# Kernel tuning notes

Measured on AMD Instinct MI355X. Metric: run time of the kernel, lower is better.

Reference implementation:

```python
import jax, jax.numpy as jnp
import numpy as np

N_SITES = 100000
N_PERM = 6
N_NEIGH = 6
FEAT = 64
OUT_FEAT = 64


def setup_inputs() -> dict:
    key = jax.random.key(0)
    k1, k2, k3, k4 = jax.random.split(key, 4)
    X_sites = jax.random.normal(k1, (N_SITES, FEAT), dtype=jnp.float32)
    X_NSs = jax.random.randint(k2, (N_SITES, N_PERM, N_NEIGH), 0, N_SITES, dtype=jnp.int64)
    # Linear(input_feature=N_NEIGH*FEAT, output_feature=OUT_FEAT): weight (out, in), bias (out,)
    W = jax.random.normal(k3, (OUT_FEAT, N_NEIGH * FEAT), dtype=jnp.float32) * (1.0 / np.sqrt(N_NEIGH * FEAT))
    b = jax.random.normal(k4, (OUT_FEAT,), dtype=jnp.float32) * 0.01
    return {"X_sites": X_sites, "X_NSs": X_NSs, "N_sites": N_SITES, "W": W, "b": b}


def reference(X_sites, X_NSs, N_sites, W, b):
    # Vectorized form of the per-site Python loop:
    # for each site i: gather X_sites[X_NSs[i]] -> (P, n_neigh, feat),
    # flatten to (P, n_neigh*feat), apply Linear.
    N, P, n = X_NSs.shape
    f = X_sites.shape[1]
    gathered = X_sites[X_NSs]                      # (N, P, n, f)  irregular gather
    flat = gathered.reshape(N, P, n * f)           # (N, P, n*f)
    # Linear: y = x @ W.T + b
    out = jnp.einsum('npi,oi->npo', flat, W) + b   # (N, P, out)
    return out
```

## Files before the change

### kernel.cpp

```cpp
#include <hip/hip_runtime.h>
#include <hip/hip_fp16.h>

#define FEAT   64
#define NNEIGH 6
#define OUTF   64
#define INFEAT (NNEIGH * FEAT)

typedef __attribute__((ext_vector_type(8))) short bf16x8;
typedef __attribute__((ext_vector_type(4))) float f32x4;

__device__ __forceinline__ short bf16_hi(float v) {
  return (short)(__float_as_uint(v) >> 16);
}
__device__ __forceinline__ float bf16_rec(float v) {
  return __uint_as_float(__float_as_uint(v) & 0xffff0000u);
}

__global__ __launch_bounds__(256) void lcnn_prep(
    const float* __restrict__ W, short* __restrict__ BThi,
    short* __restrict__ BTlo) {
  const int t = blockIdx.x * 256 + threadIdx.x;
  if (t >= INFEAT * FEAT) return;
  const int j = t >> 6, f = t & 63;
  const float v = W[(size_t)(j & 63) * INFEAT + (j >> 6) * 64 + f];
  const short h = bf16_hi(v);
  const float lo = v - bf16_rec(v);
  BThi[t] = h;
  BTlo[t] = bf16_hi(lo);
}

__global__ __launch_bounds__(256) void lcnn_p1_mfma(
    const float* __restrict__ X, const short* __restrict__ BThi,
    const short* __restrict__ BTlo, __half* __restrict__ Y, int nsites) {
  __shared__ alignas(16) __half lds[4][16 * INFEAT];

  const int lane = threadIdx.x & 63;
  const int wid  = threadIdx.x >> 6;
  const int g    = lane >> 4;
  const int c    = lane & 15;
  const int m0   = (blockIdx.x * 4 + wid) * 16;

  int srow = m0 + c;
  if (srow >= nsites) srow = nsites - 1;
  const float* xr = X + (size_t)srow * FEAT;

  float af[2][8];
  *(float4*)&af[0][0] = *(const float4*)(xr + g * 8);
  *(float4*)&af[0][4] = *(const float4*)(xr + g * 8 + 4);
  *(float4*)&af[1][0] = *(const float4*)(xr + 32 + g * 8);
  *(float4*)&af[1][4] = *(const float4*)(xr + 32 + g * 8 + 4);

  bf16x8 ah[2], al[2];
#pragma unroll
  for (int ks = 0; ks < 2; ++ks)
#pragma unroll
    for (int i = 0; i < 8; ++i) {
      const float v = af[ks][i];
      ah[ks][i] = bf16_hi(v);
      al[ks][i] = bf16_hi(v - bf16_rec(v));
    }

#pragma unroll 4
  for (int nt = 0; nt < 24; ++nt) {
    const int jrow = (nt * 16 + c) * 64;
    const bf16x8 bh0 = *(const bf16x8*)(BThi + jrow + g * 8);
    const bf16x8 bh1 = *(const bf16x8*)(BThi + jrow + 32 + g * 8);
    const bf16x8 bl0 = *(const bf16x8*)(BTlo + jrow + g * 8);
    const bf16x8 bl1 = *(const bf16x8*)(BTlo + jrow + 32 + g * 8);

    f32x4 acc = {0.f, 0.f, 0.f, 0.f};
    acc = __builtin_amdgcn_mfma_f32_16x16x32_bf16(ah[0], bh0, acc, 0, 0, 0);
    acc = __builtin_amdgcn_mfma_f32_16x16x32_bf16(al[0], bh0, acc, 0, 0, 0);
    acc = __builtin_amdgcn_mfma_f32_16x16x32_bf16(ah[0], bl0, acc, 0, 0, 0);
    acc = __builtin_amdgcn_mfma_f32_16x16x32_bf16(ah[1], bh1, acc, 0, 0, 0);
    acc = __builtin_amdgcn_mfma_f32_16x16x32_bf16(al[1], bh1, acc, 0, 0, 0);
    acc = __builtin_amdgcn_mfma_f32_16x16x32_bf16(ah[1], bl1, acc, 0, 0, 0);

#pragma unroll
    for (int r = 0; r < 4; ++r)
      lds[wid][(g * 4 + r) * INFEAT + nt * 16 + c] = __float2half(acc[r]);
  }

  const int rows = min(16, nsites - m0);
  if (rows > 0) {
    const int n16 = rows * 48;
    const uint4* src = (const uint4*)&lds[wid][0];
    uint4* dst = (uint4*)((char*)Y + (size_t)m0 * (INFEAT * 2));
    for (int t = lane; t < n16; t += 64) dst[t] = src[t];
  }
}

__global__ __launch_bounds__(256) void lcnn_phase2(
    const int* __restrict__ idx, const __half* __restrict__ Y,
    const float* __restrict__ b, float* __restrict__ out, int nrows) {
  const int lane = threadIdx.x & 63;
  int row = blockIdx.x * 4 + (threadIdx.x >> 6);
  if (row >= nrows) return;
  row = __builtin_amdgcn_readfirstlane(row);

  const int* ip = idx + (size_t)row * NNEIGH;
  const int s0 = ip[0], s1 = ip[1], s2 = ip[2], s3 = ip[3], s4 = ip[4], s5 = ip[5];

  const __half y0 = Y[(size_t)s0 * INFEAT + 0 * FEAT + lane];
  const __half y1 = Y[(size_t)s1 * INFEAT + 1 * FEAT + lane];
  const __half y2 = Y[(size_t)s2 * INFEAT + 2 * FEAT + lane];
  const __half y3 = Y[(size_t)s3 * INFEAT + 3 * FEAT + lane];
  const __half y4 = Y[(size_t)s4 * INFEAT + 4 * FEAT + lane];
  const __half y5 = Y[(size_t)s5 * INFEAT + 5 * FEAT + lane];

  const float acc = b[lane]
      + ((__half2float(y0) + __half2float(y1)) + (__half2float(y2) + __half2float(y3)))
      + (__half2float(y4) + __half2float(y5));

  __builtin_nontemporal_store(acc, &out[(size_t)row * OUTF + lane]);
}

__global__ __launch_bounds__(256) void lcnn_naive(
    const float* __restrict__ X, const int* __restrict__ idx,
    const float* __restrict__ W, const float* __restrict__ b,
    float* __restrict__ out, int nrows) {
  const int lane = threadIdx.x & 63;
  int row = blockIdx.x * 4 + (threadIdx.x >> 6);
  if (row >= nrows) return;

  const int* ip = idx + (size_t)row * NNEIGH;
  float acc = b[lane];
#pragma unroll 1
  for (int k = 0; k < NNEIGH; ++k) {
    const int s = ip[k];
    const float* xr = X + (size_t)s * FEAT;
    const float* wr = W + (size_t)lane * INFEAT + k * FEAT;
#pragma unroll
    for (int f = 0; f < FEAT; ++f) acc += xr[f] * wr[f];
  }
  out[(size_t)row * OUTF + lane] = acc;
}

extern "C" void kernel_launch(void* const* d_in, const int* in_sizes, int n_in,
                              void* d_out, int out_size, void* d_ws, size_t ws_size,
                              hipStream_t stream) {
  const float* X   = (const float*)d_in[0];
  const int*   idx = (const int*)d_in[1];
  const float* W   = (const float*)d_in[3];
  const float* b   = (const float*)d_in[4];
  float*       out = (float*)d_out;

  const int nsites = in_sizes[0] / FEAT;
  const int nrows  = in_sizes[1] / NNEIGH;

  const size_t ybytes  = (size_t)nsites * INFEAT * sizeof(__half);
  const size_t btbytes = (size_t)INFEAT * FEAT * sizeof(short);
  if (ws_size >= ybytes + 2 * btbytes) {
    __half* Y    = (__half*)d_ws;
    short*  BThi = (short*)((char*)d_ws + ybytes);
    short*  BTlo = BThi + INFEAT * FEAT;

    lcnn_prep<<<(INFEAT * FEAT + 255) / 256, 256, 0, stream>>>(W, BThi, BTlo);
    lcnn_p1_mfma<<<(nsites + 63) / 64, 256, 0, stream>>>(X, BThi, BTlo, Y, nsites);
    lcnn_phase2<<<(nrows + 3) / 4, 256, 0, stream>>>(idx, Y, b, out, nrows);
  } else {
    lcnn_naive<<<(nrows + 3) / 4, 256, 0, stream>>>(X, idx, W, b, out, nrows);
  }
}
```

Measured before the change: 361.3 us.

## Drop LDS staging in projection kernel and batch gather rows per wave

The MFMA projection kernel swaps operand order so each lane holds four consecutive output columns of one site row. It then writes them straight to Y as 8-byte stores, removing the LDS staging buffer and the copy-out loop. The gather/sum kernel now has each wave handle 8 output rows. It loads all 48 indices with one coalesced load, shares them via shuffles, and issues 24 independent 4-byte half2 gathers per lane before summing. This aims for more memory-level parallelism and wider stores, in exchange for narrower, less-coalesced Y writes in the first kernel.

```diff
diff --git a/kernel.cpp b/kernel.cpp
--- a/kernel.cpp
+++ b/kernel.cpp
@@ -23,17 +23,13 @@
   if (t >= INFEAT * FEAT) return;
   const int j = t >> 6, f = t & 63;
   const float v = W[(size_t)(j & 63) * INFEAT + (j >> 6) * 64 + f];
-  const short h = bf16_hi(v);
-  const float lo = v - bf16_rec(v);
-  BThi[t] = h;
-  BTlo[t] = bf16_hi(lo);
+  BThi[t] = bf16_hi(v);
+  BTlo[t] = bf16_hi(v - bf16_rec(v));
 }
 
 __global__ __launch_bounds__(256) void lcnn_p1_mfma(
     const float* __restrict__ X, const short* __restrict__ BThi,
     const short* __restrict__ BTlo, __half* __restrict__ Y, int nsites) {
-  __shared__ alignas(16) __half lds[4][16 * INFEAT];
-
   const int lane = threadIdx.x & 63;
   const int wid  = threadIdx.x >> 6;
   const int g    = lane >> 4;
@@ -41,7 +37,8 @@
   const int m0   = (blockIdx.x * 4 + wid) * 16;
 
   int srow = m0 + c;
-  if (srow >= nsites) srow = nsites - 1;
+  const bool valid = (srow < nsites);
+  if (!valid) srow = nsites - 1;
   const float* xr = X + (size_t)srow * FEAT;
 
   float af[2][8];
@@ -50,14 +47,14 @@
   *(float4*)&af[1][0] = *(const float4*)(xr + 32 + g * 8);
   *(float4*)&af[1][4] = *(const float4*)(xr + 32 + g * 8 + 4);
 
-  bf16x8 ah[2], al[2];
+  bf16x8 xh[2], xl[2];
 #pragma unroll
   for (int ks = 0; ks < 2; ++ks)
 #pragma unroll
     for (int i = 0; i < 8; ++i) {
       const float v = af[ks][i];
-      ah[ks][i] = bf16_hi(v);
-      al[ks][i] = bf16_hi(v - bf16_rec(v));
+      xh[ks][i] = bf16_hi(v);
+      xl[ks][i] = bf16_hi(v - bf16_rec(v));
     }
 
 #pragma unroll 4
@@ -69,24 +66,18 @@
     const bf16x8 bl1 = *(const bf16x8*)(BTlo + jrow + 32 + g * 8);
 
     f32x4 acc = {0.f, 0.f, 0.f, 0.f};
-    acc = __builtin_amdgcn_mfma_f32_16x16x32_bf16(ah[0], bh0, acc, 0, 0, 0);
-    acc = __builtin_amdgcn_mfma_f32_16x16x32_bf16(al[0], bh0, acc, 0, 0, 0);
-    acc = __builtin_amdgcn_mfma_f32_16x16x32_bf16(ah[0], bl0, acc, 0, 0, 0);
-    acc = __builtin_amdgcn_mfma_f32_16x16x32_bf16(ah[1], bh1, acc, 0, 0, 0);
-    acc = __builtin_amdgcn_mfma_f32_16x16x32_bf16(al[1], bh1, acc, 0, 0, 0);
-    acc = __builtin_amdgcn_mfma_f32_16x16x32_bf16(ah[1], bl1, acc, 0, 0, 0);
+    acc = __builtin_amdgcn_mfma_f32_16x16x32_bf16(bh0, xh[0], acc, 0, 0, 0);
+    acc = __builtin_amdgcn_mfma_f32_16x16x32_bf16(bh0, xl[0], acc, 0, 0, 0);
+    acc = __builtin_amdgcn_mfma_f32_16x16x32_bf16(bl0, xh[0], acc, 0, 0, 0);
+    acc = __builtin_amdgcn_mfma_f32_16x16x32_bf16(bh1, xh[1], acc, 0, 0, 0);
+    acc = __builtin_amdgcn_mfma_f32_16x16x32_bf16(bh1, xl[1], acc, 0, 0, 0);
+    acc = __builtin_amdgcn_mfma_f32_16x16x32_bf16(bl1, xh[1], acc, 0, 0, 0);
 
+    union { __half h[4]; uint2 u; } p;
 #pragma unroll
-    for (int r = 0; r < 4; ++r)
-      lds[wid][(g * 4 + r) * INFEAT + nt * 16 + c] = __float2half(acc[r]);
-  }
-
-  const int rows = min(16, nsites - m0);
-  if (rows > 0) {
-    const int n16 = rows * 48;
-    const uint4* src = (const uint4*)&lds[wid][0];
-    uint4* dst = (uint4*)((char*)Y + (size_t)m0 * (INFEAT * 2));
-    for (int t = lane; t < n16; t += 64) dst[t] = src[t];
+    for (int r = 0; r < 4; ++r) p.h[r] = __float2half(acc[r]);
+    if (valid)
+      *(uint2*)(Y + (size_t)srow * INFEAT + nt * 16 + g * 4) = p.u;
   }
 }
 
@@ -94,25 +85,43 @@
     const int* __restrict__ idx, const __half* __restrict__ Y,
     const float* __restrict__ b, float* __restrict__ out, int nrows) {
   const int lane = threadIdx.x & 63;
-  int row = blockIdx.x * 4 + (threadIdx.x >> 6);
-  if (row >= nrows) return;
-  row = __builtin_amdgcn_readfirstlane(row);
+  const int wid  = threadIdx.x >> 6;
+  const int l32  = lane & 31;
+  const int h    = lane >> 5;
+  const int rowbase = (blockIdx.x * 4 + wid) * 8;
+  if (rowbase >= nrows) return;
 
-  const int* ip = idx + (size_t)row * NNEIGH;
-  const int s0 = ip[0], s1 = ip[1], s2 = ip[2], s3 = ip[3], s4 = ip[4], s5 = ip[5];
+  const int tmax = nrows * NNEIGH - 1;
+  const int iv = idx[min(rowbase * NNEIGH + min(lane, 47), tmax)];
 
-  const __half y0 = Y[(size_t)s0 * INFEAT + 0 * FEAT + lane];
-  const __half y1 = Y[(size_t)s1 * INFEAT + 1 * FEAT + lane];
-  const __half y2 = Y[(size_t)s2 * INFEAT + 2 * FEAT + lane];
-  const __half y3 = Y[(size_t)s3 * INFEAT + 3 * FEAT + lane];
-  const __half y4 = Y[(size_t)s4 * INFEAT + 4 * FEAT + lane];
-  const __half y5 = Y[(size_t)s5 * INFEAT + 5 * FEAT + lane];
+  const float2 bb = *(const float2*)(b + l32 * 2);
+  const char* Yb = (const char*)Y;
 
-  const float acc = b[lane]
-      + ((__half2float(y0) + __half2float(y1)) + (__half2float(y2) + __half2float(y3)))
-      + (__half2float(y4) + __half2float(y5));
+  uint u[4][6];
+#pragma unroll
+  for (int rp = 0; rp < 4; ++rp) {
+    const int r6 = (rp * 2 + h) * NNEIGH;
+#pragma unroll
+    for (int k = 0; k < NNEIGH; ++k) {
+      const int s = __shfl(iv, r6 + k);
+      u[rp][k] = *(const uint*)(Yb + ((size_t)s * (INFEAT * 2) + k * 128 + l32 * 4));
+    }
+  }
 
-  __builtin_nontemporal_store(acc, &out[(size_t)row * OUTF + lane]);
+#pragma unroll
+  for (int rp = 0; rp < 4; ++rp) {
+    float2 a = bb;
+#pragma unroll
+    for (int k = 0; k < NNEIGH; ++k) {
+      const __half2 hh = *(const __half2*)&u[rp][k];
+      const float2 f = __half22float2(hh);
+      a.x += f.x;
+      a.y += f.y;
+    }
+    const int row = rowbase + rp * 2 + h;
+    if (row < nrows)
+      *(float2*)(out + (size_t)row * OUTF + l32 * 2) = a;
+  }
 }
 
 __global__ __launch_bounds__(256) void lcnn_naive(
@@ -157,7 +166,7 @@
 
     lcnn_prep<<<(INFEAT * FEAT + 255) / 256, 256, 0, stream>>>(W, BThi, BTlo);
     lcnn_p1_mfma<<<(nsites + 63) / 64, 256, 0, stream>>>(X, BThi, BTlo, Y, nsites);
-    lcnn_phase2<<<(nrows + 3) / 4, 256, 0, stream>>>(idx, Y, b, out, nrows);
+    lcnn_phase2<<<(nrows + 31) / 32, 256, 0, stream>>>(idx, Y, b, out, nrows);
   } else {
     lcnn_naive<<<(nrows + 3) / 4, 256, 0, stream>>>(X, idx, W, b, out, nrows);
   }
```

Measured after the change: 332.0 us. 8.1% less time.
